# Kernel tuning notes

Measured on AMD Instinct MI355X. Metric: run time of the kernel, lower is better.

## Reference

```python
import jax, jax.numpy as jnp
import numpy as np


def setup_inputs() -> dict:
    key = jax.random.key(0)
    k1, k2, k3 = jax.random.split(key, 3)
    B, L, D = 4, 2056, 1024  # L = K + T = 8 + 2048
    x = jax.random.normal(k1, (B, L, D), dtype=jnp.float32)
    # Linear weights stored as (in_features, out_features); no bias (config.bias=False)
    W_attn = jax.random.normal(k2, (D, 3 * D), dtype=jnp.float32) * 0.02
    W_proj = jax.random.normal(k3, (D, D), dtype=jnp.float32) * 0.02
    return {"x": x, "W_attn": W_attn, "W_proj": W_proj, "n_head": 16, "n_memory": 8}


def reference(x, W_attn, W_proj, n_head, n_memory):
    B, L, C = x.shape
    K = n_memory
    T = L - K
    hd = C // n_head
    scale = 1.0 / np.sqrt(hd).astype(np.float32)

    qkv = x @ W_attn                      # (B, L, 3C)
    q, k, v = jnp.split(qkv, 3, axis=2)
    # (B, H, L, hd)
    q = q.reshape(B, L, n_head, hd).transpose(0, 2, 1, 3)
    k = k.reshape(B, L, n_head, hd).transpose(0, 2, 1, 3)
    v = v.reshape(B, L, n_head, hd).transpose(0, 2, 1, 3)

    att = jnp.einsum("bhqd,bhkd->bhqk", q, k) * scale  # (B, H, L, L)

    # Mask: all-True except the (seq x seq) block which is causal (lower-tri).
    # Memory rows (first K) attend everywhere; seq rows attend to all memory + causal seq.
    mask = jnp.ones((L, L), dtype=bool)
    seq_causal = jnp.tril(jnp.ones((T, T), dtype=bool))
    mask = mask.at[K:, K:].set(seq_causal)

    att = jnp.where(mask[None, None, :, :], att, jnp.float32(-jnp.inf))
    att = jax.nn.softmax(att, axis=-1)

    y = jnp.einsum("bhqk,bhkd->bhqd", att, v)  # (B, H, L, hd)
    y = y.transpose(0, 2, 1, 3).reshape(B, L, C)
    return y @ W_proj
```

## Files before the change

### kernel.cpp

```cpp
#include <hip/hip_runtime.h>
#include <hip/hip_bf16.h>
#include <hip/hip_fp16.h>

typedef _Float16 f16x8 __attribute__((ext_vector_type(8)));
typedef _Float16 f16x4 __attribute__((ext_vector_type(4)));
typedef float f32x4 __attribute__((ext_vector_type(4)));

typedef const __attribute__((address_space(1))) void gvoid_t;
typedef __attribute__((address_space(3))) void svoid_t;

constexpr int Bb = 4, Lq = 2056, Dd = 1024, NH = 16, HD = 64, NMEM = 8;
constexpr int Mtot = Bb * Lq;
constexpr int KEYS = 64;
constexpr int NT = (Lq + KEYS - 1) / KEYS;
constexpr int NTQP = 17;

__device__ inline float fexp2(float x) {
  float r;
  asm("v_exp_f32 %0, %1" : "=v"(r) : "v"(x));
  return r;
}

__global__ __launch_bounds__(256) void cast_f16(const float* __restrict__ in,
                                                _Float16* __restrict__ out, int n8) {
  int i = blockIdx.x * blockDim.x + threadIdx.x;
  if (i >= n8) return;
  const float4* p = reinterpret_cast<const float4*>(in) + (size_t)i * 2;
  float4 a = p[0], b = p[1];
  f16x8 o;
  o[0] = (_Float16)a.x; o[1] = (_Float16)a.y; o[2] = (_Float16)a.z; o[3] = (_Float16)a.w;
  o[4] = (_Float16)b.x; o[5] = (_Float16)b.y; o[6] = (_Float16)b.z; o[7] = (_Float16)b.w;
  *(reinterpret_cast<f16x8*>(out) + i) = o;
}

__global__ void transpose_cast(const float* __restrict__ in, _Float16* __restrict__ out,
                               int rows, int cols) {
  __shared__ float t[32][33];
  int c0 = blockIdx.x * 32, r0 = blockIdx.y * 32;
  int tx = threadIdx.x, ty = threadIdx.y;
#pragma unroll
  for (int i = 0; i < 4; ++i)
    t[ty + i * 8][tx] = in[(size_t)(r0 + ty + i * 8) * cols + c0 + tx];
  __syncthreads();
#pragma unroll
  for (int i = 0; i < 4; ++i)
    out[(size_t)(c0 + ty + i * 8) * rows + r0 + tx] = (_Float16)t[tx][ty + i * 8];
}

template <int EPI>
__global__ __launch_bounds__(256) void gemm_f16(
    const _Float16* __restrict__ A, const _Float16* __restrict__ Bt,
    int M, int N, int Kd, float* __restrict__ Cf,
    _Float16* __restrict__ qout, _Float16* __restrict__ kout, _Float16* __restrict__ vtout) {
  constexpr int BM = 128, BN = 128, BK = 64;
  __shared__ _Float16 smem[2][2 * BM * BK];
  const int tid = threadIdx.x;
  const int wid = tid >> 6, lane = tid & 63;
  const int wr = wid >> 1, wc = wid & 1;
  const int l16 = lane & 15, lq = lane >> 4;

  const int gx = gridDim.x;
  const int nwg = gx * gridDim.y;
  const int i0 = blockIdx.y * gx + blockIdx.x;
  const int cpx = nwg >> 3;
  const int logical = (i0 & 7) * cpx + (i0 >> 3);
  const int m0 = (logical / gx) * BM, n0 = (logical % gx) * BN;

  f32x4 acc[4][4];
#pragma unroll
  for (int i = 0; i < 4; ++i)
#pragma unroll
    for (int j = 0; j < 4; ++j) acc[i][j] = (f32x4){0.f, 0.f, 0.f, 0.f};

  auto stage = [&](int sb, int kt) {
    const size_t kbase = (size_t)kt * BK;
    _Float16* sm = smem[sb];
#pragma unroll
    for (int c = 0; c < 4; ++c) {
      int q = wid * 256 + c * 64 + lane;
      int r = q >> 3, cc = q & 7;
      int gr = m0 + r; gr = gr < M ? gr : M - 1;
      const _Float16* src = A + (size_t)gr * Kd + kbase + ((cc ^ (r & 7)) << 3);
      __builtin_amdgcn_global_load_lds((gvoid_t*)src,
          (svoid_t*)(sm + (size_t)(wid * 256 + c * 64) * 8), 16, 0, 0);
    }
#pragma unroll
    for (int c = 0; c < 4; ++c) {
      int q = wid * 256 + c * 64 + lane;
      int r = q >> 3, cc = q & 7;
      const _Float16* src = Bt + (size_t)(n0 + r) * Kd + kbase + ((cc ^ (r & 7)) << 3);
      __builtin_amdgcn_global_load_lds((gvoid_t*)src,
          (svoid_t*)(sm + BM * BK + (size_t)(wid * 256 + c * 64) * 8), 16, 0, 0);
    }
  };

  const int KT = Kd / BK;
  stage(0, 0);
  __syncthreads();
  int sbuf = 0;
  for (int kt = 0; kt < KT; ++kt) {
    if (kt + 1 < KT) stage(sbuf ^ 1, kt + 1);
    const _Float16* sm = smem[sbuf];
#pragma unroll
    for (int kk = 0; kk < 2; ++kk) {
      f16x8 af[4], bfr[4];
#pragma unroll
      for (int i = 0; i < 4; ++i) {
        int r = wr * 64 + i * 16 + l16;
        int off = r * 64 + (((kk * 4 + lq) ^ (r & 7)) << 3);
        af[i] = *(const f16x8*)(sm + off);
      }
#pragma unroll
      for (int j = 0; j < 4; ++j) {
        int r = wc * 64 + j * 16 + l16;
        int off = BM * BK + r * 64 + (((kk * 4 + lq) ^ (r & 7)) << 3);
        bfr[j] = *(const f16x8*)(sm + off);
      }
#pragma unroll
      for (int i = 0; i < 4; ++i)
#pragma unroll
        for (int j = 0; j < 4; ++j)
          acc[i][j] = __builtin_amdgcn_mfma_f32_16x16x32_f16(af[i], bfr[j], acc[i][j], 0, 0, 0);
    }
    __syncthreads();
    sbuf ^= 1;
  }

  if (EPI == 1 && n0 >= 2 * Dd) {
#pragma unroll
    for (int i = 0; i < 4; ++i) {
      int mb = m0 + wr * 64 + i * 16 + lq * 4;
      if (mb >= M) continue;
      int b = mb / Lq, l = mb - b * Lq;
#pragma unroll
      for (int j = 0; j < 4; ++j) {
        int n = n0 + wc * 64 + j * 16 + l16;
        int h = (n >> 6) & 15, d = n & 63;
        if (l + 4 <= Lq) {
          f16x4 pk;
          pk[0] = (_Float16)acc[i][j][0]; pk[1] = (_Float16)acc[i][j][1];
          pk[2] = (_Float16)acc[i][j][2]; pk[3] = (_Float16)acc[i][j][3];
          *(f16x4*)(vtout + ((size_t)(b * NH + h) * HD + d) * Lq + l) = pk;
        } else {
#pragma unroll
          for (int r = 0; r < 4; ++r) {
            int m = mb + r;
            if (m >= M) continue;
            int b2 = m / Lq, l2 = m - b2 * Lq;
            vtout[((size_t)(b2 * NH + h) * HD + d) * Lq + l2] = (_Float16)acc[i][j][r];
          }
        }
      }
    }
  } else {
#pragma unroll
    for (int i = 0; i < 4; ++i) {
#pragma unroll
      for (int r = 0; r < 4; ++r) {
        int m = m0 + wr * 64 + i * 16 + lq * 4 + r;
        if (m >= M) continue;
        if (EPI == 0) {
#pragma unroll
          for (int j = 0; j < 4; ++j) {
            int n = n0 + wc * 64 + j * 16 + l16;
            Cf[(size_t)m * N + n] = acc[i][j][r];
          }
        } else {
          int b = m / Lq, l = m - b * Lq;
#pragma unroll
          for (int j = 0; j < 4; ++j) {
            int n = n0 + wc * 64 + j * 16 + l16;
            int which = n >> 10, h = (n >> 6) & 15, d = n & 63;
            int bh = b * NH + h;
            _Float16 v = (_Float16)acc[i][j][r];
            if (which == 0)
              qout[((size_t)bh * Lq + l) * HD + d] = v;
            else
              kout[((size_t)bh * Lq + l) * HD + d] = v;
          }
        }
      }
    }
  }
}

__global__ __launch_bounds__(256) void attn_f16(const _Float16* __restrict__ qm,
                                                const _Float16* __restrict__ km,
                                                const _Float16* __restrict__ vt,
                                                _Float16* __restrict__ y) {
  __shared__ _Float16 kvs[2][2][KEYS * HD];

  const int i0 = blockIdx.y * (int)gridDim.x + blockIdx.x;
  const int logical = (i0 & 7) * (NTQP * Bb * NH / 8) + (i0 >> 3);
  const int bh = logical / NTQP;
  const int px = logical % NTQP;

  const int wid = threadIdx.x >> 6, lane = threadIdx.x & 63;
  const int l16 = lane & 15, lq = lane >> 4;

  const _Float16* qbase = qm + (size_t)bh * Lq * HD;
  const _Float16* kbase = km + (size_t)bh * Lq * HD;
  const _Float16* vbase = vt + (size_t)bh * HD * Lq;
  const int b = bh >> 4, h = bh & 15;

  const _Float16 QSC = (_Float16)(0.125f * 1.44269504f);

  f16x8 ones;
#pragma unroll
  for (int e = 0; e < 8; ++e) ones[e] = (_Float16)1.0f;

  const int nseg = (px == 0) ? 1 : 2;
  for (int seg = 0; seg < nseg; ++seg) {
    const int qt = (px == 0) ? 0 : (seg == 0 ? NT - px : px);
    const int qr0 = qt * 64 + wid * 16;

    int qrow = qr0 + l16; if (qrow > Lq - 1) qrow = Lq - 1;
    f16x8 qf0 = *(const f16x8*)(qbase + (size_t)qrow * HD + lq * 8);
    f16x8 qf1 = *(const f16x8*)(qbase + (size_t)qrow * HD + 32 + lq * 8);
#pragma unroll
    for (int e = 0; e < 8; ++e) {
      qf0[e] *= QSC;
      qf1[e] *= QSC;
    }

    const int irow = qr0 + l16;
    const int kmax = (irow < NMEM) ? (Lq - 1) : (irow < Lq - 1 ? irow : Lq - 1);

    f32x4 o[4];
#pragma unroll
    for (int dt = 0; dt < 4; ++dt) o[dt] = (f32x4){0.f, 0.f, 0.f, 0.f};
    f32x4 ol = (f32x4){0.f, 0.f, 0.f, 0.f};

    const int ntiles = (qt == 0) ? NT : (qt + 1 < NT ? qt + 1 : NT);

    auto stage = [&](int sb, int t) {
      const int j0 = t * KEYS;
#pragma unroll
      for (int c = 0; c < 2; ++c) {
        const int q = (wid * 2 + c) * 64 + lane;
        const int row = q >> 3, cc = q & 7;
        int key = j0 + row; if (key > Lq - 1) key = Lq - 1;
        const _Float16* srcK = kbase + (size_t)key * HD + ((cc ^ (row & 7)) << 3);
        __builtin_amdgcn_global_load_lds((gvoid_t*)srcK,
            (svoid_t*)(&kvs[sb][0][(size_t)(wid * 2 + c) * 512]), 16, 0, 0);
        int kc = j0 + ((cc ^ (row & 7)) << 3);
        if (kc + 8 > Lq) kc = Lq - 8;
        const _Float16* srcV = vbase + (size_t)row * Lq + kc;
        __builtin_amdgcn_global_load_lds((gvoid_t*)srcV,
            (svoid_t*)(&kvs[sb][1][(size_t)(wid * 2 + c) * 512]), 16, 0, 0);
      }
    };

    stage(0, 0);
    __syncthreads();
    int buf = 0;
    for (int t = 0; t < ntiles; ++t) {
      if (t + 1 < ntiles) stage(buf ^ 1, t + 1);
      const int j0 = t * KEYS;
      const bool fastw = ((t + 1) * KEYS <= qr0);
      const _Float16* Kl = &kvs[buf][0][0];
      const _Float16* Vl = &kvs[buf][1][0];
#pragma unroll
      for (int ks = 0; ks < 2; ++ks) {
        const int r0 = ks * 32 + l16, r1 = r0 + 16;
        f16x8 ka0 = *(const f16x8*)(Kl + r0 * 64 + ((lq ^ (r0 & 7)) << 3));
        f16x8 kb0 = *(const f16x8*)(Kl + r0 * 64 + (((4 + lq) ^ (r0 & 7)) << 3));
        f16x8 ka1 = *(const f16x8*)(Kl + r1 * 64 + ((lq ^ (r1 & 7)) << 3));
        f16x8 kb1 = *(const f16x8*)(Kl + r1 * 64 + (((4 + lq) ^ (r1 & 7)) << 3));
        f32x4 s0 = (f32x4){0.f, 0.f, 0.f, 0.f};
        f32x4 s1 = (f32x4){0.f, 0.f, 0.f, 0.f};
        __builtin_amdgcn_s_setprio(1);
        s0 = __builtin_amdgcn_mfma_f32_16x16x32_f16(ka0, qf0, s0, 0, 0, 0);
        s0 = __builtin_amdgcn_mfma_f32_16x16x32_f16(kb0, qf1, s0, 0, 0, 0);
        s1 = __builtin_amdgcn_mfma_f32_16x16x32_f16(ka1, qf0, s1, 0, 0, 0);
        s1 = __builtin_amdgcn_mfma_f32_16x16x32_f16(kb1, qf1, s1, 0, 0, 0);
        __builtin_amdgcn_s_setprio(0);

        f16x8 pf;
        if (fastw) {
#pragma unroll
          for (int r = 0; r < 4; ++r) {
            pf[r] = (_Float16)fexp2(s0[r]);
            pf[4 + r] = (_Float16)fexp2(s1[r]);
          }
        } else {
          const int kb0i = j0 + ks * 32 + lq * 4;
#pragma unroll
          for (int r = 0; r < 4; ++r) {
            pf[r] = (kb0i + r <= kmax) ? (_Float16)fexp2(s0[r]) : (_Float16)0.f;
            pf[4 + r] = (kb0i + 16 + r <= kmax) ? (_Float16)fexp2(s1[r]) : (_Float16)0.f;
          }
        }

        __builtin_amdgcn_s_setprio(1);
        ol = __builtin_amdgcn_mfma_f32_16x16x32_f16(pf, ones, ol, 0, 0, 0);
#pragma unroll
        for (int dt = 0; dt < 4; ++dt) {
          const int vr = dt * 16 + l16;
          const int g0 = ks * 4 + (lq >> 1);
          const int wo = (lq & 1) * 4;
          f16x4 v0 = *(const f16x4*)(Vl + vr * 64 + ((g0 ^ (vr & 7)) << 3) + wo);
          f16x4 v1 = *(const f16x4*)(Vl + vr * 64 + (((g0 + 2) ^ (vr & 7)) << 3) + wo);
          f16x8 vf;
#pragma unroll
          for (int e = 0; e < 4; ++e) { vf[e] = v0[e]; vf[4 + e] = v1[e]; }
          o[dt] = __builtin_amdgcn_mfma_f32_16x16x32_f16(pf, vf, o[dt], 0, 0, 0);
        }
        __builtin_amdgcn_s_setprio(0);
      }
      __syncthreads();
      buf ^= 1;
    }

#pragma unroll
    for (int r = 0; r < 4; ++r) {
      int orow = qr0 + lq * 4 + r;
      if (orow >= Lq) continue;
      float inv = 1.0f / ol[r];
#pragma unroll
      for (int dt = 0; dt < 4; ++dt)
        y[((size_t)(b * Lq + orow)) * Dd + h * HD + dt * 16 + l16] = (_Float16)(o[dt][r] * inv);
    }
  }
}

extern "C" void kernel_launch(void* const* d_in, const int* in_sizes, int n_in,
                              void* d_out, int out_size, void* d_ws, size_t ws_size,
                              hipStream_t stream) {
  (void)in_sizes; (void)n_in; (void)out_size; (void)ws_size;
  const float* x = (const float*)d_in[0];
  const float* W_attn = (const float*)d_in[1];
  const float* W_proj = (const float*)d_in[2];
  float* out = (float*)d_out;

  char* w = (char*)d_ws;
  _Float16* xh  = (_Float16*)(w);
  _Float16* wta = (_Float16*)(w + 16842752);
  _Float16* wtp = (_Float16*)(w + 23134208);
  _Float16* qh  = (_Float16*)(w + 25231360);
  _Float16* kh  = (_Float16*)(w + 42074112);
  _Float16* vth = (_Float16*)(w + 58916864);
  _Float16* yh  = xh;

  cast_f16<<<dim3((Mtot * Dd) / 8 / 256), dim3(256), 0, stream>>>(x, xh, (Mtot * Dd) / 8);
  transpose_cast<<<dim3(3 * Dd / 32, Dd / 32), dim3(32, 8), 0, stream>>>(W_attn, wta, Dd, 3 * Dd);
  transpose_cast<<<dim3(Dd / 32, Dd / 32), dim3(32, 8), 0, stream>>>(W_proj, wtp, Dd, Dd);

  gemm_f16<1><<<dim3(3 * Dd / 128, (Mtot + 127) / 128), dim3(256), 0, stream>>>(
      xh, wta, Mtot, 3 * Dd, Dd, nullptr, qh, kh, vth);

  attn_f16<<<dim3(NTQP, Bb * NH), dim3(256), 0, stream>>>(qh, kh, vth, yh);

  gemm_f16<0><<<dim3(Dd / 128, (Mtot + 127) / 128), dim3(256), 0, stream>>>(
      yh, wtp, Mtot, Dd, Dd, out, nullptr, nullptr, nullptr);
}
```

Measured before the change: 216.0 us.

## Pre-permute V-transpose columns so attention reads V fragments with one vector load

The QKV GEMM epilogue now writes V-transposed with a padded row stride and columns permuted inside each 64-key block, so the attention kernel can load each V MFMA operand as a single 8-wide LDS read instead of two 4-wide reads plus a shuffle. The K/V staging is rewritten with precomputed pointers that advance per tile and a separate clamped path for the last tile. The double-buffer loop is manually unrolled so buffer addresses are compile-time constants. The permuted layout couples the producer epilogue and the consumer, which makes both harder to keep in sync.

```diff
diff --git a/kernel.cpp b/kernel.cpp
--- a/kernel.cpp
+++ b/kernel.cpp
@@ -14,6 +14,7 @@
 constexpr int KEYS = 64;
 constexpr int NT = (Lq + KEYS - 1) / KEYS;
 constexpr int NTQP = 17;
+constexpr int LqV = 2064;
 
 __device__ inline float fexp2(float x) {
   float r;
@@ -137,17 +138,23 @@
         int n = n0 + wc * 64 + j * 16 + l16;
         int h = (n >> 6) & 15, d = n & 63;
         if (l + 4 <= Lq) {
+          int kk = l & 63;
+          int ks = kk >> 5, rem = kk & 31, half = rem >> 4, idx = rem & 15;
+          int col = (l & ~63) + (ks * 4 + (idx >> 2)) * 8 + half * 4;
           f16x4 pk;
           pk[0] = (_Float16)acc[i][j][0]; pk[1] = (_Float16)acc[i][j][1];
           pk[2] = (_Float16)acc[i][j][2]; pk[3] = (_Float16)acc[i][j][3];
-          *(f16x4*)(vtout + ((size_t)(b * NH + h) * HD + d) * Lq + l) = pk;
+          *(f16x4*)(vtout + ((size_t)(b * NH + h) * HD + d) * LqV + col) = pk;
         } else {
 #pragma unroll
           for (int r = 0; r < 4; ++r) {
             int m = mb + r;
             if (m >= M) continue;
             int b2 = m / Lq, l2 = m - b2 * Lq;
-            vtout[((size_t)(b2 * NH + h) * HD + d) * Lq + l2] = (_Float16)acc[i][j][r];
+            int kk = l2 & 63;
+            int ks = kk >> 5, rem = kk & 31, half = rem >> 4, idx = rem & 15;
+            int col = (l2 & ~63) + (ks * 4 + (idx >> 2)) * 8 + half * 4 + (idx & 3);
+            vtout[((size_t)(b2 * NH + h) * HD + d) * LqV + col] = (_Float16)acc[i][j][r];
           }
         }
       }
@@ -188,7 +195,8 @@
                                                 const _Float16* __restrict__ km,
                                                 const _Float16* __restrict__ vt,
                                                 _Float16* __restrict__ y) {
-  __shared__ _Float16 kvs[2][2][KEYS * HD];
+  __shared__ _Float16 kls[2][KEYS * HD];
+  __shared__ _Float16 vls[2][KEYS * HD];
 
   const int i0 = blockIdx.y * (int)gridDim.x + blockIdx.x;
   const int logical = (i0 & 7) * (NTQP * Bb * NH / 8) + (i0 >> 3);
@@ -200,7 +208,7 @@
 
   const _Float16* qbase = qm + (size_t)bh * Lq * HD;
   const _Float16* kbase = km + (size_t)bh * Lq * HD;
-  const _Float16* vbase = vt + (size_t)bh * HD * Lq;
+  const _Float16* vbase = vt + (size_t)bh * HD * LqV;
   const int b = bh >> 4, h = bh & 15;
 
   const _Float16 QSC = (_Float16)(0.125f * 1.44269504f);
@@ -208,6 +216,16 @@
   f16x8 ones;
 #pragma unroll
   for (int e = 0; e < 8; ++e) ones[e] = (_Float16)1.0f;
+
+  const int qA = (wid * 2 + 0) * 64 + lane, qB = (wid * 2 + 1) * 64 + lane;
+  const int rA = qA >> 3, cA = qA & 7;
+  const int rB = qB >> 3, cB = qB & 7;
+  const int ofA = (cA ^ (rA & 7)) << 3;
+  const int ofB = (cB ^ (rB & 7)) << 3;
+  _Float16* dKA0 = &kls[0][(wid * 2 + 0) * 512]; _Float16* dKB0 = &kls[0][(wid * 2 + 1) * 512];
+  _Float16* dKA1 = &kls[1][(wid * 2 + 0) * 512]; _Float16* dKB1 = &kls[1][(wid * 2 + 1) * 512];
+  _Float16* dVA0 = &vls[0][(wid * 2 + 0) * 512]; _Float16* dVB0 = &vls[0][(wid * 2 + 1) * 512];
+  _Float16* dVA1 = &vls[1][(wid * 2 + 0) * 512]; _Float16* dVB1 = &vls[1][(wid * 2 + 1) * 512];
 
   const int nseg = (px == 0) ? 1 : 2;
   for (int seg = 0; seg < nseg; ++seg) {
@@ -233,33 +251,37 @@
 
     const int ntiles = (qt == 0) ? NT : (qt + 1 < NT ? qt + 1 : NT);
 
-    auto stage = [&](int sb, int t) {
-      const int j0 = t * KEYS;
-#pragma unroll
-      for (int c = 0; c < 2; ++c) {
-        const int q = (wid * 2 + c) * 64 + lane;
-        const int row = q >> 3, cc = q & 7;
-        int key = j0 + row; if (key > Lq - 1) key = Lq - 1;
-        const _Float16* srcK = kbase + (size_t)key * HD + ((cc ^ (row & 7)) << 3);
-        __builtin_amdgcn_global_load_lds((gvoid_t*)srcK,
-            (svoid_t*)(&kvs[sb][0][(size_t)(wid * 2 + c) * 512]), 16, 0, 0);
-        int kc = j0 + ((cc ^ (row & 7)) << 3);
-        if (kc + 8 > Lq) kc = Lq - 8;
-        const _Float16* srcV = vbase + (size_t)row * Lq + kc;
-        __builtin_amdgcn_global_load_lds((gvoid_t*)srcV,
-            (svoid_t*)(&kvs[sb][1][(size_t)(wid * 2 + c) * 512]), 16, 0, 0);
-      }
+    const _Float16* pkA = kbase + (size_t)rA * HD + ofA;
+    const _Float16* pkB = kbase + (size_t)rB * HD + ofB;
+    const _Float16* pvA = vbase + (size_t)rA * LqV + ofA;
+    const _Float16* pvB = vbase + (size_t)rB * LqV + ofB;
+
+    auto stage_fast = [&](_Float16* dK0, _Float16* dK1, _Float16* dV0, _Float16* dV1) {
+      __builtin_amdgcn_global_load_lds((gvoid_t*)pkA, (svoid_t*)dK0, 16, 0, 0);
+      __builtin_amdgcn_global_load_lds((gvoid_t*)pkB, (svoid_t*)dK1, 16, 0, 0);
+      __builtin_amdgcn_global_load_lds((gvoid_t*)pvA, (svoid_t*)dV0, 16, 0, 0);
+      __builtin_amdgcn_global_load_lds((gvoid_t*)pvB, (svoid_t*)dV1, 16, 0, 0);
+      pkA += KEYS * HD; pkB += KEYS * HD; pvA += KEYS; pvB += KEYS;
     };
-
-    stage(0, 0);
-    __syncthreads();
-    int buf = 0;
-    for (int t = 0; t < ntiles; ++t) {
-      if (t + 1 < ntiles) stage(buf ^ 1, t + 1);
+    auto stage_clamp = [&](_Float16* dK0, _Float16* dK1, _Float16* dV0, _Float16* dV1) {
+      int keyA = 2048 + rA; if (keyA > Lq - 1) keyA = Lq - 1;
+      int keyB = 2048 + rB; if (keyB > Lq - 1) keyB = Lq - 1;
+      __builtin_amdgcn_global_load_lds((gvoid_t*)(kbase + (size_t)keyA * HD + ofA),
+                                       (svoid_t*)dK0, 16, 0, 0);
+      __builtin_amdgcn_global_load_lds((gvoid_t*)(kbase + (size_t)keyB * HD + ofB),
+                                       (svoid_t*)dK1, 16, 0, 0);
+      int kcA = 2048 + ofA; if (kcA + 8 > LqV) kcA = LqV - 8;
+      int kcB = 2048 + ofB; if (kcB + 8 > LqV) kcB = LqV - 8;
+      __builtin_amdgcn_global_load_lds((gvoid_t*)(vbase + (size_t)rA * LqV + kcA),
+                                       (svoid_t*)dV0, 16, 0, 0);
+      __builtin_amdgcn_global_load_lds((gvoid_t*)(vbase + (size_t)rB * LqV + kcB),
+                                       (svoid_t*)dV1, 16, 0, 0);
+    };
+
+    auto compute = [&](const _Float16* Kl, const _Float16* Vl, int t) {
       const int j0 = t * KEYS;
       const bool fastw = ((t + 1) * KEYS <= qr0);
-      const _Float16* Kl = &kvs[buf][0][0];
-      const _Float16* Vl = &kvs[buf][1][0];
+      const int lim = kmax - j0;
 #pragma unroll
       for (int ks = 0; ks < 2; ++ks) {
         const int r0 = ks * 32 + l16, r1 = r0 + 16;
@@ -284,11 +306,11 @@
             pf[4 + r] = (_Float16)fexp2(s1[r]);
           }
         } else {
-          const int kb0i = j0 + ks * 32 + lq * 4;
+          const int kb = ks * 32 + lq * 4;
 #pragma unroll
           for (int r = 0; r < 4; ++r) {
-            pf[r] = (kb0i + r <= kmax) ? (_Float16)fexp2(s0[r]) : (_Float16)0.f;
-            pf[4 + r] = (kb0i + 16 + r <= kmax) ? (_Float16)fexp2(s1[r]) : (_Float16)0.f;
+            pf[r] = (kb + r <= lim) ? (_Float16)fexp2(s0[r]) : (_Float16)0.f;
+            pf[4 + r] = (kb + 16 + r <= lim) ? (_Float16)fexp2(s1[r]) : (_Float16)0.f;
           }
         }
 
@@ -297,19 +319,38 @@
 #pragma unroll
         for (int dt = 0; dt < 4; ++dt) {
           const int vr = dt * 16 + l16;
-          const int g0 = ks * 4 + (lq >> 1);
-          const int wo = (lq & 1) * 4;
-          f16x4 v0 = *(const f16x4*)(Vl + vr * 64 + ((g0 ^ (vr & 7)) << 3) + wo);
-          f16x4 v1 = *(const f16x4*)(Vl + vr * 64 + (((g0 + 2) ^ (vr & 7)) << 3) + wo);
-          f16x8 vf;
-#pragma unroll
-          for (int e = 0; e < 4; ++e) { vf[e] = v0[e]; vf[4 + e] = v1[e]; }
+          const int g = ks * 4 + lq;
+          f16x8 vf = *(const f16x8*)(Vl + vr * 64 + ((g ^ (vr & 7)) << 3));
           o[dt] = __builtin_amdgcn_mfma_f32_16x16x32_f16(pf, vf, o[dt], 0, 0, 0);
         }
         __builtin_amdgcn_s_setprio(0);
       }
+    };
+
+    stage_fast(dKA0, dKB0, dVA0, dVB0);
+    __syncthreads();
+    int t = 0;
+    for (;;) {
+      {
+        int nxt = t + 1;
+        if (nxt < ntiles) {
+          if (nxt == NT - 1) stage_clamp(dKA1, dKB1, dVA1, dVB1);
+          else stage_fast(dKA1, dKB1, dVA1, dVB1);
+        }
+      }
+      compute(kls[0], vls[0], t);
       __syncthreads();
-      buf ^= 1;
+      if (++t >= ntiles) break;
+      {
+        int nxt = t + 1;
+        if (nxt < ntiles) {
+          if (nxt == NT - 1) stage_clamp(dKA0, dKB0, dVA0, dVB0);
+          else stage_fast(dKA0, dKB0, dVA0, dVB0);
+        }
+      }
+      compute(kls[1], vls[1], t);
+      __syncthreads();
+      if (++t >= ntiles) break;
     }
 
 #pragma unroll
```

Result: faster. 204.7 us (-5.2%).
